# Optimization experiments

Hardware: AMD Instinct MI355X
Metric: run time of the kernel (lower is better)

The kernel has to match this reference:

```python
import jax, jax.numpy as jnp
import numpy as np

EMBED_DIM = 1024
NUM_HEADS = 16
HEAD_DIM = EMBED_DIM // NUM_HEADS
B, S = 4, 4096


def maxpool1d_2(x):
    # MaxPooling1D(pool_size=2, strides=2, padding='same'); seq len is even so no padding needed.
    n, l, d = x.shape
    return jnp.max(x.reshape(n, l // 2, 2, d), axis=2)


def setup_inputs() -> dict:
    key = jax.random.key(0)
    ks = jax.random.split(key, 5)
    scale = 1.0 / np.sqrt(EMBED_DIM)
    return {
        "x": jax.random.normal(ks[0], (B, S, EMBED_DIM), dtype=jnp.float32),
        "Wq": jax.random.normal(ks[1], (EMBED_DIM, EMBED_DIM), dtype=jnp.float32) * scale,
        "bq": jnp.zeros((EMBED_DIM,), dtype=jnp.float32),
        "Wk": jax.random.normal(ks[2], (EMBED_DIM, EMBED_DIM), dtype=jnp.float32) * scale,
        "bk": jnp.zeros((EMBED_DIM,), dtype=jnp.float32),
        "Wv": jax.random.normal(ks[3], (EMBED_DIM, EMBED_DIM), dtype=jnp.float32) * scale,
        "bv": jnp.zeros((EMBED_DIM,), dtype=jnp.float32),
        "Wo": jax.random.normal(ks[4], (EMBED_DIM, EMBED_DIM), dtype=jnp.float32) * scale,
        "bo": jnp.zeros((EMBED_DIM,), dtype=jnp.float32),
    }


def _separate_heads_pool(x, batch_size):
    # [B, S, E] -> [B, S, H, hd] -> [B, H, S, hd] -> [B*H, S, hd] -> pooled [B*H, S/2, hd]
    n, s, _ = x.shape
    x = x.reshape(batch_size, s, NUM_HEADS, HEAD_DIM).transpose(0, 2, 1, 3)
    x = x.reshape(batch_size * NUM_HEADS, s, HEAD_DIM)
    return maxpool1d_2(x)


def reference(x, Wq, bq, Wk, bk, Wv, bv, Wo, bo):
    batch_size = x.shape[0]
    q = x @ Wq + bq
    k = x @ Wk + bk
    v = x @ Wv + bv
    q = _separate_heads_pool(q, batch_size)  # [B*H, S/2, hd]
    k = _separate_heads_pool(k, batch_size)
    v = _separate_heads_pool(v, batch_size)
    score = jnp.einsum('nqd,nkd->nqk', q, k) / jnp.sqrt(jnp.float32(HEAD_DIM))
    weights = jax.nn.softmax(score, axis=-1)
    attn = jnp.einsum('nqk,nkd->nqd', weights, v)  # [B*H, S/2, hd]
    attn = maxpool1d_2(attn)  # [B*H, S/4, hd]
    # reshape back: (batch, -1, head_dim*num_heads). NOTE: original reshapes
    # [B*H, S/4, hd] directly to (B, -1, E) without transposing heads back,
    # so we replicate that exact layout.
    attn = attn.reshape(batch_size, -1, HEAD_DIM * NUM_HEADS)  # [B, S/4 (head-major mix), E]
    return attn @ Wo + bo
```

## Files before the change

kernel.cpp:

```cpp
#include <hip/hip_runtime.h>
#include <stdint.h>

typedef __attribute__((ext_vector_type(8))) __bf16 bf16x8;
typedef __attribute__((ext_vector_type(4))) float f32x4;
typedef __attribute__((ext_vector_type(8))) int i32x8;

#define DEV __device__ __forceinline__

DEV unsigned short f2bf(float f) {
  union { float f; uint32_t u; } v; v.f = f;
  return (unsigned short)((v.u + 0x7fffu + ((v.u >> 16) & 1u)) >> 16);
}

DEV uint32_t pk2bf(float lo, float hi) {
  union { float f; uint32_t u; } a, b;
  a.f = lo; b.f = hi;
  return __builtin_amdgcn_perm(b.u + 0x8000u, a.u + 0x8000u, 0x07060302u);
}

DEV void gld16(const void* g, void* l) {
  __builtin_amdgcn_global_load_lds(
      (const __attribute__((address_space(1))) uint32_t*)g,
      (__attribute__((address_space(3))) uint32_t*)l, 16, 0, 0);
}

union Frag8 { i32x8 v; uint4 q[2]; };

__global__ __launch_bounds__(256) void k_cvt_x(const float* __restrict__ x,
                                               uint8_t* __restrict__ x8) {
  size_t t = (size_t)blockIdx.x * 256 + threadIdx.x;
  const float4* xv = (const float4*)x;
  float4 a = xv[t * 2], b = xv[t * 2 + 1];
  int lo = 0, hi = 0;
  lo = __builtin_amdgcn_cvt_pk_fp8_f32(a.x, a.y, lo, false);
  lo = __builtin_amdgcn_cvt_pk_fp8_f32(a.z, a.w, lo, true);
  hi = __builtin_amdgcn_cvt_pk_fp8_f32(b.x, b.y, hi, false);
  hi = __builtin_amdgcn_cvt_pk_fp8_f32(b.z, b.w, hi, true);
  int2 pk; pk.x = lo; pk.y = hi;
  *(int2*)&x8[t * 8] = pk;
}

__global__ void k_cvt_w(const float* __restrict__ W0, const float* __restrict__ W1,
                        const float* __restrict__ W2, const float* __restrict__ W3,
                        uint8_t* __restrict__ W8, unsigned short* __restrict__ WoT) {
  const int z = blockIdx.z;
  const float* W = (z == 0) ? W0 : (z == 1) ? W1 : (z == 2) ? W2 : W3;
  __shared__ float tile[32][33];
  const int n0 = blockIdx.x * 32, k0 = blockIdx.y * 32;
  const int tx = threadIdx.x, ty = threadIdx.y;
  const int tid = ty * 32 + tx;
#pragma unroll
  for (int i = 0; i < 4; i++)
    tile[ty * 4 + i][tx] = W[(size_t)(k0 + ty * 4 + i) * 1024 + n0 + tx];
  __syncthreads();
  if (z < 3) {
    int nn = tid >> 3, kg = tid & 7;
    int w_ = 0;
    w_ = __builtin_amdgcn_cvt_pk_fp8_f32(32.f * tile[kg * 4 + 0][nn],
                                         32.f * tile[kg * 4 + 1][nn], w_, false);
    w_ = __builtin_amdgcn_cvt_pk_fp8_f32(32.f * tile[kg * 4 + 2][nn],
                                         32.f * tile[kg * 4 + 3][nn], w_, true);
    *(uint32_t*)&W8[(size_t)z * 1048576 + (size_t)(n0 + nn) * 1024 + k0 + kg * 4] =
        (uint32_t)w_;
  } else {
#pragma unroll
    for (int i = 0; i < 4; i++)
      WoT[(size_t)(n0 + ty * 4 + i) * 1024 + k0 + tx] = f2bf(tile[tx][ty * 4 + i]);
  }
}

__global__ __launch_bounds__(256) void k_gemm_qkv(
    const uint8_t* __restrict__ A, const uint8_t* __restrict__ W8,
    const float* __restrict__ bq, const float* __restrict__ bk,
    const float* __restrict__ bv,
    unsigned short* __restrict__ Qp, unsigned short* __restrict__ Kp,
    unsigned short* __restrict__ Vt) {
  const int tid = threadIdx.x;
  const int n0 = blockIdx.x * 128, m0 = blockIdx.y * 128;
  const int z = blockIdx.z;
  const uint8_t* Bt = W8 + (size_t)z * 1048576;
  const float* bias = (z == 0) ? bq : (z == 1) ? bk : bv;

  __shared__ __align__(16) uint8_t lA[128 * 128];
  __shared__ __align__(16) uint8_t lB[128 * 128];

  const int lane = tid & 63, w = tid >> 6;
  const int wr = w >> 1, wc = w & 1;
  const int r = lane & 15, qd = lane >> 4;
  const int rl = lane >> 3, sg = lane & 7;

  f32x4 acc[4][4];
#pragma unroll
  for (int i = 0; i < 4; i++)
#pragma unroll
    for (int j = 0; j < 4; j++) acc[i][j] = (f32x4){0.f, 0.f, 0.f, 0.f};

  for (int k0 = 0; k0 < 1024; k0 += 128) {
    __syncthreads();
#pragma unroll
    for (int p = 0; p < 4; p++) {
      int row = (p * 4 + w) * 8 + rl;
      int g = sg ^ (row & 7);
      gld16(&A[(size_t)(m0 + row) * 1024 + k0 + g * 16], &lA[row * 128 + sg * 16]);
      gld16(&Bt[(size_t)(n0 + row) * 1024 + k0 + g * 16], &lB[row * 128 + sg * 16]);
    }
    __syncthreads();
    Frag8 bfr[4];
#pragma unroll
    for (int nt = 0; nt < 4; nt++) {
      int row = wc * 64 + nt * 16 + r;
      int g0 = (2 * qd) ^ (row & 7), g1 = (2 * qd + 1) ^ (row & 7);
      bfr[nt].q[0] = *(const uint4*)&lB[row * 128 + g0 * 16];
      bfr[nt].q[1] = *(const uint4*)&lB[row * 128 + g1 * 16];
    }
#pragma unroll
    for (int mt = 0; mt < 4; mt++) {
      int row = wr * 64 + mt * 16 + r;
      int g0 = (2 * qd) ^ (row & 7), g1 = (2 * qd + 1) ^ (row & 7);
      Frag8 af;
      af.q[0] = *(const uint4*)&lA[row * 128 + g0 * 16];
      af.q[1] = *(const uint4*)&lA[row * 128 + g1 * 16];
#pragma unroll
      for (int nt = 0; nt < 4; nt++)
        acc[mt][nt] = __builtin_amdgcn_mfma_scale_f32_16x16x128_f8f6f4(
            af.v, bfr[nt].v, acc[mt][nt], 0, 0, 0, 0x7f7f7f7f, 0, 0x7f7f7f7f);
    }
  }

  unsigned short* OP = (z == 0) ? Qp : Kp;
#pragma unroll
  for (int nt = 0; nt < 4; nt++) {
    int n = n0 + wc * 64 + nt * 16 + r;
    float bv_ = bias[n];
    int h = n >> 6, d = n & 63;
#pragma unroll
    for (int mt = 0; mt < 4; mt++) {
      int mg = m0 + wr * 64 + mt * 16 + qd * 4;
      int b = mg >> 12, s2 = (mg & 4095) >> 1;
      int bh = b * 16 + h;
      f32x4 a = acc[mt][nt];
      float v0 = fmaxf(a.x, a.y) * 0.03125f + bv_;
      float v1 = fmaxf(a.z, a.w) * 0.03125f + bv_;
      if (z == 2) {
        uint32_t pk = (uint32_t)f2bf(v0) | ((uint32_t)f2bf(v1) << 16);
        *(uint32_t*)&Vt[((size_t)bh * 64 + d) * 2048 + s2] = pk;
      } else {
        size_t base = ((size_t)bh * 2048 + s2) * 64 + d;
        OP[base] = f2bf(v0);
        OP[base + 64] = f2bf(v1);
      }
    }
  }
}

__global__ __launch_bounds__(256) void k_gemm_out(
    const unsigned short* __restrict__ A, const unsigned short* __restrict__ Bt,
    const float* __restrict__ bias, float* __restrict__ fout) {
  const int tid = threadIdx.x;
  const int n0 = blockIdx.x * 128, m0 = blockIdx.y * 128;

  __shared__ __align__(16) unsigned short lA[128 * 64];
  __shared__ __align__(16) unsigned short lB[128 * 64];

  const int lane = tid & 63, w = tid >> 6;
  const int wr = w >> 1, wc = w & 1;
  const int r = lane & 15, qd = lane >> 4;
  const int srow = tid >> 3, sg = tid & 7;

  f32x4 acc[4][4];
#pragma unroll
  for (int i = 0; i < 4; i++)
#pragma unroll
    for (int j = 0; j < 4; j++) acc[i][j] = (f32x4){0.f, 0.f, 0.f, 0.f};

  for (int k0 = 0; k0 < 1024; k0 += 64) {
    __syncthreads();
#pragma unroll
    for (int p = 0; p < 4; p++) {
      int row = p * 32 + srow;
      int gs = sg ^ (row & 7);
      gld16(&A[(size_t)(m0 + row) * 1024 + k0 + gs * 8], &lA[row * 64 + sg * 8]);
      gld16(&Bt[(size_t)(n0 + row) * 1024 + k0 + gs * 8], &lB[row * 64 + sg * 8]);
    }
    __syncthreads();
#pragma unroll
    for (int kf = 0; kf < 2; kf++) {
      bf16x8 af[4], bfr[4];
#pragma unroll
      for (int mt = 0; mt < 4; mt++) {
        int row = wr * 64 + mt * 16 + r;
        int lg = (kf * 4 + qd) ^ (row & 7);
        af[mt] = *(const bf16x8*)&lA[row * 64 + lg * 8];
      }
#pragma unroll
      for (int nt = 0; nt < 4; nt++) {
        int row = wc * 64 + nt * 16 + r;
        int lg = (kf * 4 + qd) ^ (row & 7);
        bfr[nt] = *(const bf16x8*)&lB[row * 64 + lg * 8];
      }
#pragma unroll
      for (int mt = 0; mt < 4; mt++)
#pragma unroll
        for (int nt = 0; nt < 4; nt++)
          acc[mt][nt] = __builtin_amdgcn_mfma_f32_16x16x32_bf16(af[mt], bfr[nt],
                                                               acc[mt][nt], 0, 0, 0);
    }
  }

#pragma unroll
  for (int nt = 0; nt < 4; nt++) {
    int n = n0 + wc * 64 + nt * 16 + r;
    float bv = bias[n];
#pragma unroll
    for (int mt = 0; mt < 4; mt++) {
      int mg = m0 + wr * 64 + mt * 16 + qd * 4;
      f32x4 a = acc[mt][nt];
      fout[(size_t)(mg + 0) * 1024 + n] = a.x + bv;
      fout[(size_t)(mg + 1) * 1024 + n] = a.y + bv;
      fout[(size_t)(mg + 2) * 1024 + n] = a.z + bv;
      fout[(size_t)(mg + 3) * 1024 + n] = a.w + bv;
    }
  }
}

__global__ __launch_bounds__(256) void k_attn(const unsigned short* __restrict__ Qp,
                                              const unsigned short* __restrict__ Kp,
                                              const unsigned short* __restrict__ Vt,
                                              unsigned short* __restrict__ Am) {
  const int tid = threadIdx.x;
  const int qt = blockIdx.x, bh = blockIdx.y;
  const int w = tid >> 6, lane = tid & 63;
  const int r = lane & 15, qd = lane >> 4;
  const int srow = tid >> 3, sg = tid & 7;

  __shared__ __align__(16) unsigned short lK[64 * 64];
  __shared__ __align__(16) unsigned short lV[64 * 64];
  __shared__ __align__(16) unsigned short lP[4][16 * 80];

  const int q0 = qt * 64;
  const int qrow = q0 + w * 16 + r;
  const size_t qbase = ((size_t)bh * 2048 + qrow) * 64;
  const bf16x8 bq0 = *(const bf16x8*)&Qp[qbase + qd * 8];
  const bf16x8 bq1 = *(const bf16x8*)&Qp[qbase + 32 + qd * 8];

  const unsigned short* Kg = Kp + (size_t)bh * 2048 * 64;
  const unsigned short* Vg = Vt + (size_t)bh * 64 * 2048;

  const float K2 = 0.125f * 1.44269504f;

  float lsum = 0.f;
  f32x4 accO[4];
#pragma unroll
  for (int i = 0; i < 4; i++) accO[i] = (f32x4){0.f, 0.f, 0.f, 0.f};

  char* lPw = (char*)&lP[w][0];

  for (int kb = 0; kb < 2048; kb += 64) {
    __syncthreads();
#pragma unroll
    for (int c = 0; c < 2; c++) {
      int row = c * 32 + srow;
      int gs = sg ^ (row & 7);
      gld16(&Kg[(size_t)(kb + row) * 64 + gs * 8], &lK[row * 64 + sg * 8]);
      gld16(&Vg[(size_t)row * 2048 + kb + gs * 8], &lV[row * 64 + sg * 8]);
    }
    __syncthreads();

    f32x4 s[4];
#pragma unroll
    for (int mt = 0; mt < 4; mt++) {
      int row = mt * 16 + r;
      int lg0 = qd ^ (row & 7), lg1 = (4 + qd) ^ (row & 7);
      bf16x8 ak0 = *(const bf16x8*)&lK[row * 64 + lg0 * 8];
      bf16x8 ak1 = *(const bf16x8*)&lK[row * 64 + lg1 * 8];
      s[mt] = (f32x4){0.f, 0.f, 0.f, 0.f};
      s[mt] = __builtin_amdgcn_mfma_f32_16x16x32_bf16(ak0, bq0, s[mt], 0, 0, 0);
      s[mt] = __builtin_amdgcn_mfma_f32_16x16x32_bf16(ak1, bq1, s[mt], 0, 0, 0);
    }

#pragma unroll
    for (int mt = 0; mt < 4; mt++) {
      float p0 = __builtin_amdgcn_exp2f(fmaf(s[mt][0], K2, -0.5f));
      float p1 = __builtin_amdgcn_exp2f(fmaf(s[mt][1], K2, -0.5f));
      float p2 = __builtin_amdgcn_exp2f(fmaf(s[mt][2], K2, -0.5f));
      float p3 = __builtin_amdgcn_exp2f(fmaf(s[mt][3], K2, -0.5f));
      lsum += (p0 + p1) + (p2 + p3);
      uint2 dw; dw.x = pk2bf(p0, p1); dw.y = pk2bf(p2, p3);
      int off = r * 160 + (((2 * mt + (qd >> 1)) ^ (r & 7)) << 4) + ((qd & 1) << 3);
      *(uint2*)(lPw + off) = dw;
    }

    bf16x8 ap0 = *(const bf16x8*)(lPw + r * 160 + ((qd ^ (r & 7)) << 4));
    bf16x8 ap1 = *(const bf16x8*)(lPw + r * 160 + (((4 + qd) ^ (r & 7)) << 4));

#pragma unroll
    for (int nt = 0; nt < 4; nt++) {
      int row = nt * 16 + r;
      int lg0 = qd ^ (row & 7), lg1 = (4 + qd) ^ (row & 7);
      bf16x8 bv0 = *(const bf16x8*)&lV[row * 64 + lg0 * 8];
      bf16x8 bv1 = *(const bf16x8*)&lV[row * 64 + lg1 * 8];
      accO[nt] = __builtin_amdgcn_mfma_f32_16x16x32_bf16(ap0, bv0, accO[nt], 0, 0, 0);
      accO[nt] = __builtin_amdgcn_mfma_f32_16x16x32_bf16(ap1, bv1, accO[nt], 0, 0, 0);
    }
  }

  lsum += __shfl_xor(lsum, 16, 64);
  lsum += __shfl_xor(lsum, 32, 64);
  float linv = 1.f / lsum;
  float inv[4];
#pragma unroll
  for (int g = 0; g < 4; g++) inv[g] = __shfl(linv, qd * 4 + g, 64);

#pragma unroll
  for (int nt = 0; nt < 4; nt++) {
    int d = nt * 16 + r;
    int s4 = (q0 + w * 16 + qd * 4) >> 1;
    float o0 = fmaxf(accO[nt][0] * inv[0], accO[nt][1] * inv[1]);
    float o1 = fmaxf(accO[nt][2] * inv[2], accO[nt][3] * inv[3]);
    size_t base = ((size_t)bh * 1024 + s4) * 64 + d;
    Am[base] = f2bf(o0);
    Am[base + 64] = f2bf(o1);
  }
}

extern "C" void kernel_launch(void* const* d_in, const int* in_sizes, int n_in,
                              void* d_out, int out_size, void* d_ws, size_t ws_size,
                              hipStream_t stream) {
  const float* x  = (const float*)d_in[0];
  const float* Wq = (const float*)d_in[1];
  const float* bq = (const float*)d_in[2];
  const float* Wk = (const float*)d_in[3];
  const float* bk = (const float*)d_in[4];
  const float* Wv = (const float*)d_in[5];
  const float* bv = (const float*)d_in[6];
  const float* Wo = (const float*)d_in[7];
  const float* bo = (const float*)d_in[8];
  float* out = (float*)d_out;

  uint8_t* ws = (uint8_t*)d_ws;
  uint8_t*        x8  = ws;
  uint8_t*        W8  = ws + 16777216;
  unsigned short* WoT = (unsigned short*)(ws + 19922944);
  unsigned short* Qp  = (unsigned short*)(ws + 22020096);
  unsigned short* Kp  = (unsigned short*)(ws + 38797312);
  unsigned short* Vt  = (unsigned short*)(ws + 55574528);
  unsigned short* Am  = (unsigned short*)(ws + 72351744);

  k_cvt_x<<<8192, 256, 0, stream>>>(x, x8);
  k_cvt_w<<<dim3(32, 32, 4), dim3(32, 8), 0, stream>>>(Wq, Wk, Wv, Wo, W8, WoT);
  k_gemm_qkv<<<dim3(8, 128, 3), 256, 0, stream>>>(x8, W8, bq, bk, bv, Qp, Kp, Vt);
  k_attn<<<dim3(32, 64), 256, 0, stream>>>(Qp, Kp, Vt, Am);
  k_gemm_out<<<dim3(8, 32), 256, 0, stream>>>(Am, WoT, bo, out);
}
```

Baseline: 379.9 us.

## Double-buffer LDS tiles and swizzle block order in GEMM and attention kernels

Converts the QKV GEMM, output GEMM and attention kernels from a single LDS buffer to double buffering: the next K-tile is prefetched with global_load_lds while the current tile is consumed, and one barrier per step replaces two. It also remaps block indices to swizzle the launch order, which changes which tiles run concurrently and how they share L2, and adds a launch-bounds occupancy hint of 2. The cost is doubled shared memory per block and the risk that the async loads into the other buffer are not waited on before that buffer is read.

```diff
diff --git a/kernel.cpp b/kernel.cpp
--- a/kernel.cpp
+++ b/kernel.cpp
@@ -69,20 +69,23 @@
   }
 }
 
-__global__ __launch_bounds__(256) void k_gemm_qkv(
+__global__ __launch_bounds__(256, 2) void k_gemm_qkv(
     const uint8_t* __restrict__ A, const uint8_t* __restrict__ W8,
     const float* __restrict__ bq, const float* __restrict__ bk,
     const float* __restrict__ bv,
     unsigned short* __restrict__ Qp, unsigned short* __restrict__ Kp,
     unsigned short* __restrict__ Vt) {
   const int tid = threadIdx.x;
-  const int n0 = blockIdx.x * 128, m0 = blockIdx.y * 128;
-  const int z = blockIdx.z;
+  int flat = (blockIdx.z * 128 + blockIdx.y) * 8 + blockIdx.x;
+  int swz = (flat & 7) * 384 + (flat >> 3);
+  const int n0 = (swz & 7) * 128;
+  const int m0 = ((swz >> 3) & 127) * 128;
+  const int z = swz >> 10;
   const uint8_t* Bt = W8 + (size_t)z * 1048576;
   const float* bias = (z == 0) ? bq : (z == 1) ? bk : bv;
 
-  __shared__ __align__(16) uint8_t lA[128 * 128];
-  __shared__ __align__(16) uint8_t lB[128 * 128];
+  __shared__ __align__(16) uint8_t lA[2][128 * 128];
+  __shared__ __align__(16) uint8_t lB[2][128 * 128];
 
   const int lane = tid & 63, w = tid >> 6;
   const int wr = w >> 1, wc = w & 1;
@@ -95,37 +98,52 @@
 #pragma unroll
     for (int j = 0; j < 4; j++) acc[i][j] = (f32x4){0.f, 0.f, 0.f, 0.f};
 
-  for (int k0 = 0; k0 < 1024; k0 += 128) {
-    __syncthreads();
-#pragma unroll
-    for (int p = 0; p < 4; p++) {
-      int row = (p * 4 + w) * 8 + rl;
-      int g = sg ^ (row & 7);
-      gld16(&A[(size_t)(m0 + row) * 1024 + k0 + g * 16], &lA[row * 128 + sg * 16]);
-      gld16(&Bt[(size_t)(n0 + row) * 1024 + k0 + g * 16], &lB[row * 128 + sg * 16]);
-    }
-    __syncthreads();
+#pragma unroll
+  for (int p = 0; p < 4; p++) {
+    int row = (p * 4 + w) * 8 + rl;
+    int g = sg ^ (row & 7);
+    gld16(&A[(size_t)(m0 + row) * 1024 + g * 16], &lA[0][row * 128 + sg * 16]);
+    gld16(&Bt[(size_t)(n0 + row) * 1024 + g * 16], &lB[0][row * 128 + sg * 16]);
+  }
+  __syncthreads();
+
+  auto kstep = [&](int cb, int t) {
+    if (t < 7) {
+      int k0 = (t + 1) << 7;
+#pragma unroll
+      for (int p = 0; p < 4; p++) {
+        int row = (p * 4 + w) * 8 + rl;
+        int g = sg ^ (row & 7);
+        gld16(&A[(size_t)(m0 + row) * 1024 + k0 + g * 16],
+              &lA[cb ^ 1][row * 128 + sg * 16]);
+        gld16(&Bt[(size_t)(n0 + row) * 1024 + k0 + g * 16],
+              &lB[cb ^ 1][row * 128 + sg * 16]);
+      }
+    }
     Frag8 bfr[4];
 #pragma unroll
     for (int nt = 0; nt < 4; nt++) {
       int row = wc * 64 + nt * 16 + r;
       int g0 = (2 * qd) ^ (row & 7), g1 = (2 * qd + 1) ^ (row & 7);
-      bfr[nt].q[0] = *(const uint4*)&lB[row * 128 + g0 * 16];
-      bfr[nt].q[1] = *(const uint4*)&lB[row * 128 + g1 * 16];
+      bfr[nt].q[0] = *(const uint4*)&lB[cb][row * 128 + g0 * 16];
+      bfr[nt].q[1] = *(const uint4*)&lB[cb][row * 128 + g1 * 16];
     }
 #pragma unroll
     for (int mt = 0; mt < 4; mt++) {
       int row = wr * 64 + mt * 16 + r;
       int g0 = (2 * qd) ^ (row & 7), g1 = (2 * qd + 1) ^ (row & 7);
       Frag8 af;
-      af.q[0] = *(const uint4*)&lA[row * 128 + g0 * 16];
-      af.q[1] = *(const uint4*)&lA[row * 128 + g1 * 16];
+      af.q[0] = *(const uint4*)&lA[cb][row * 128 + g0 * 16];
+      af.q[1] = *(const uint4*)&lA[cb][row * 128 + g1 * 16];
 #pragma unroll
       for (int nt = 0; nt < 4; nt++)
         acc[mt][nt] = __builtin_amdgcn_mfma_scale_f32_16x16x128_f8f6f4(
             af.v, bfr[nt].v, acc[mt][nt], 0, 0, 0, 0x7f7f7f7f, 0, 0x7f7f7f7f);
     }
-  }
+    __syncthreads();
+  };
+
+  for (int t = 0; t < 8; t += 2) { kstep(0, t); kstep(1, t + 1); }
 
   unsigned short* OP = (z == 0) ? Qp : Kp;
 #pragma unroll
@@ -153,14 +171,16 @@
   }
 }
 
-__global__ __launch_bounds__(256) void k_gemm_out(
+__global__ __launch_bounds__(256, 2) void k_gemm_out(
     const unsigned short* __restrict__ A, const unsigned short* __restrict__ Bt,
     const float* __restrict__ bias, float* __restrict__ fout) {
   const int tid = threadIdx.x;
-  const int n0 = blockIdx.x * 128, m0 = blockIdx.y * 128;
-
-  __shared__ __align__(16) unsigned short lA[128 * 64];
-  __shared__ __align__(16) unsigned short lB[128 * 64];
+  int flat = blockIdx.y * 8 + blockIdx.x;
+  int swz = (flat & 7) * 32 + (flat >> 3);
+  const int n0 = (swz & 7) * 128, m0 = (swz >> 3) * 128;
+
+  __shared__ __align__(16) unsigned short lA[2][128 * 64];
+  __shared__ __align__(16) unsigned short lB[2][128 * 64];
 
   const int lane = tid & 63, w = tid >> 6;
   const int wr = w >> 1, wc = w & 1;
@@ -173,16 +193,28 @@
 #pragma unroll
     for (int j = 0; j < 4; j++) acc[i][j] = (f32x4){0.f, 0.f, 0.f, 0.f};
 
-  for (int k0 = 0; k0 < 1024; k0 += 64) {
-    __syncthreads();
-#pragma unroll
-    for (int p = 0; p < 4; p++) {
-      int row = p * 32 + srow;
-      int gs = sg ^ (row & 7);
-      gld16(&A[(size_t)(m0 + row) * 1024 + k0 + gs * 8], &lA[row * 64 + sg * 8]);
-      gld16(&Bt[(size_t)(n0 + row) * 1024 + k0 + gs * 8], &lB[row * 64 + sg * 8]);
-    }
-    __syncthreads();
+#pragma unroll
+  for (int p = 0; p < 4; p++) {
+    int row = p * 32 + srow;
+    int gs = sg ^ (row & 7);
+    gld16(&A[(size_t)(m0 + row) * 1024 + gs * 8], &lA[0][row * 64 + sg * 8]);
+    gld16(&Bt[(size_t)(n0 + row) * 1024 + gs * 8], &lB[0][row * 64 + sg * 8]);
+  }
+  __syncthreads();
+
+  auto kstep = [&](int cb, int t) {
+    if (t < 15) {
+      int k0 = (t + 1) << 6;
+#pragma unroll
+      for (int p = 0; p < 4; p++) {
+        int row = p * 32 + srow;
+        int gs = sg ^ (row & 7);
+        gld16(&A[(size_t)(m0 + row) * 1024 + k0 + gs * 8],
+              &lA[cb ^ 1][row * 64 + sg * 8]);
+        gld16(&Bt[(size_t)(n0 + row) * 1024 + k0 + gs * 8],
+              &lB[cb ^ 1][row * 64 + sg * 8]);
+      }
+    }
 #pragma unroll
     for (int kf = 0; kf < 2; kf++) {
       bf16x8 af[4], bfr[4];
@@ -190,13 +222,13 @@
       for (int mt = 0; mt < 4; mt++) {
         int row = wr * 64 + mt * 16 + r;
         int lg = (kf * 4 + qd) ^ (row & 7);
-        af[mt] = *(const bf16x8*)&lA[row * 64 + lg * 8];
+        af[mt] = *(const bf16x8*)&lA[cb][row * 64 + lg * 8];
       }
 #pragma unroll
       for (int nt = 0; nt < 4; nt++) {
         int row = wc * 64 + nt * 16 + r;
         int lg = (kf * 4 + qd) ^ (row & 7);
-        bfr[nt] = *(const bf16x8*)&lB[row * 64 + lg * 8];
+        bfr[nt] = *(const bf16x8*)&lB[cb][row * 64 + lg * 8];
       }
 #pragma unroll
       for (int mt = 0; mt < 4; mt++)
@@ -205,7 +237,10 @@
           acc[mt][nt] = __builtin_amdgcn_mfma_f32_16x16x32_bf16(af[mt], bfr[nt],
                                                                acc[mt][nt], 0, 0, 0);
     }
-  }
+    __syncthreads();
+  };
+
+  for (int t = 0; t < 16; t += 2) { kstep(0, t); kstep(1, t + 1); }
 
 #pragma unroll
   for (int nt = 0; nt < 4; nt++) {
@@ -228,13 +263,15 @@
                                               const unsigned short* __restrict__ Vt,
                                               unsigned short* __restrict__ Am) {
   const int tid = threadIdx.x;
-  const int qt = blockIdx.x, bh = blockIdx.y;
+  int flat = blockIdx.y * 32 + blockIdx.x;
+  int swz = (flat & 7) * 256 + (flat >> 3);
+  const int qt = swz & 31, bh = swz >> 5;
   const int w = tid >> 6, lane = tid & 63;
   const int r = lane & 15, qd = lane >> 4;
   const int srow = tid >> 3, sg = tid & 7;
 
-  __shared__ __align__(16) unsigned short lK[64 * 64];
-  __shared__ __align__(16) unsigned short lV[64 * 64];
+  __shared__ __align__(16) unsigned short lK[2][64 * 64];
+  __shared__ __align__(16) unsigned short lV[2][64 * 64];
   __shared__ __align__(16) unsigned short lP[4][16 * 80];
 
   const int q0 = qt * 64;
@@ -255,24 +292,34 @@
 
   char* lPw = (char*)&lP[w][0];
 
-  for (int kb = 0; kb < 2048; kb += 64) {
-    __syncthreads();
-#pragma unroll
-    for (int c = 0; c < 2; c++) {
-      int row = c * 32 + srow;
-      int gs = sg ^ (row & 7);
-      gld16(&Kg[(size_t)(kb + row) * 64 + gs * 8], &lK[row * 64 + sg * 8]);
-      gld16(&Vg[(size_t)row * 2048 + kb + gs * 8], &lV[row * 64 + sg * 8]);
-    }
-    __syncthreads();
+#pragma unroll
+  for (int c = 0; c < 2; c++) {
+    int row = c * 32 + srow;
+    int gs = sg ^ (row & 7);
+    gld16(&Kg[(size_t)row * 64 + gs * 8], &lK[0][row * 64 + sg * 8]);
+    gld16(&Vg[(size_t)row * 2048 + gs * 8], &lV[0][row * 64 + sg * 8]);
+  }
+  __syncthreads();
+
+  auto kstep = [&](int cb, int t) {
+    if (t < 31) {
+      int kn = (t + 1) << 6;
+#pragma unroll
+      for (int c = 0; c < 2; c++) {
+        int row = c * 32 + srow;
+        int gs = sg ^ (row & 7);
+        gld16(&Kg[(size_t)(kn + row) * 64 + gs * 8], &lK[cb ^ 1][row * 64 + sg * 8]);
+        gld16(&Vg[(size_t)row * 2048 + kn + gs * 8], &lV[cb ^ 1][row * 64 + sg * 8]);
+      }
+    }
 
     f32x4 s[4];
 #pragma unroll
     for (int mt = 0; mt < 4; mt++) {
       int row = mt * 16 + r;
       int lg0 = qd ^ (row & 7), lg1 = (4 + qd) ^ (row & 7);
-      bf16x8 ak0 = *(const bf16x8*)&lK[row * 64 + lg0 * 8];
-      bf16x8 ak1 = *(const bf16x8*)&lK[row * 64 + lg1 * 8];
+      bf16x8 ak0 = *(const bf16x8*)&lK[cb][row * 64 + lg0 * 8];
+      bf16x8 ak1 = *(const bf16x8*)&lK[cb][row * 64 + lg1 * 8];
       s[mt] = (f32x4){0.f, 0.f, 0.f, 0.f};
       s[mt] = __builtin_amdgcn_mfma_f32_16x16x32_bf16(ak0, bq0, s[mt], 0, 0, 0);
       s[mt] = __builtin_amdgcn_mfma_f32_16x16x32_bf16(ak1, bq1, s[mt], 0, 0, 0);
@@ -297,12 +344,15 @@
     for (int nt = 0; nt < 4; nt++) {
       int row = nt * 16 + r;
       int lg0 = qd ^ (row & 7), lg1 = (4 + qd) ^ (row & 7);
-      bf16x8 bv0 = *(const bf16x8*)&lV[row * 64 + lg0 * 8];
-      bf16x8 bv1 = *(const bf16x8*)&lV[row * 64 + lg1 * 8];
+      bf16x8 bv0 = *(const bf16x8*)&lV[cb][row * 64 + lg0 * 8];
+      bf16x8 bv1 = *(const bf16x8*)&lV[cb][row * 64 + lg1 * 8];
       accO[nt] = __builtin_amdgcn_mfma_f32_16x16x32_bf16(ap0, bv0, accO[nt], 0, 0, 0);
       accO[nt] = __builtin_amdgcn_mfma_f32_16x16x32_bf16(ap1, bv1, accO[nt], 0, 0, 0);
     }
-  }
+    __syncthreads();
+  };
+
+  for (int t = 0; t < 32; t += 2) { kstep(0, t); kstep(1, t + 1); }
 
   lsum += __shfl_xor(lsum, 16, 64);
   lsum += __shfl_xor(lsum, 32, 64);
```

Result: slower. 717.7 us (+88.9%).
